# Kernel optimization log

Hardware: AMD Instinct MI355X
Metric: run time of the kernel (lower is better)

Reference implementation:

```python
import jax, jax.numpy as jnp
import numpy as np

EPS = 1e-12  # torch F.normalize eps
SIGMA_RBF = 1.0  # rbf bandwidth (init arg sigma=1)


def _l2norm(v, axis=-1):
    return v / jnp.maximum(jnp.linalg.norm(v, axis=axis, keepdims=True), EPS)


def setup_inputs() -> dict:
    key = jax.random.key(0)
    kx, kw, kb, ku, kc = jax.random.split(key, 5)
    B, C, E, F = 512, 100, 2048, 128
    x = jax.random.normal(kx, (B, E), dtype=jnp.float32)
    # per-class Linear weights [C, F, E] and biases [C, F] (torch Linear layout: out x in)
    bound = 1.0 / np.sqrt(E)
    W = jax.random.uniform(kw, (C, F, E), minval=-bound, maxval=bound, dtype=jnp.float32)
    b = jax.random.uniform(kb, (C, F), minval=-bound, maxval=bound, dtype=jnp.float32)
    # spectral-norm power-iteration vectors u (one per class, normalized)
    u = _l2norm(jax.random.normal(ku, (C, F), dtype=jnp.float32))
    # centroid buffer c (EMA means; randn stand-in for a trained state)
    c = jax.random.normal(kc, (C, F), dtype=jnp.float32)
    return {"x": x, "W": W, "b": b, "u": u, "c": c}


def reference(x, W, b, u, c):
    # --- spectral norm: one power-iteration step per class (torch default) ---
    v = _l2norm(jnp.einsum('cfe,cf->ce', W, u))        # v = normalize(W^T u)  [C,E]
    u2 = _l2norm(jnp.einsum('cfe,ce->cf', W, v))       # u = normalize(W v)    [C,F]
    sigma = jnp.einsum('cf,cfe,ce->c', u2, W, v)       # sigma = u^T W v       [C]
    Wn = W / sigma[:, None, None]
    # --- fused per-class linear projections: z[b,c,f] ---
    z = jnp.einsum('be,cfe->bcf', x, Wn) + b[None, :, :]
    # --- RBF to centroids: exp(-||c - z||^2 / (2 sigma^2)) ---
    dist2 = jnp.sum((c[None, :, :] - z) ** 2, axis=-1)  # [B, C]
    probs = jnp.exp(-dist2 / (2.0 * SIGMA_RBF ** 2))
    return probs
```

## Files before the change

### kernel.cpp

```cpp
#include <hip/hip_runtime.h>
#include <math.h>

#define B_ 512
#define C_ 100
#define E_ 2048
#define F_ 128
#define NCHUNK 16
#define CHUNKW 128

typedef _Float16 f16x8 __attribute__((ext_vector_type(8)));
typedef float    f32x4 __attribute__((ext_vector_type(4)));

#define AS1q __attribute__((address_space(1)))
#define AS3q __attribute__((address_space(3)))

__device__ __forceinline__ void gl_lds16(const void* g, void* lds_base) {
    __builtin_amdgcn_global_load_lds((const AS1q void*)g, (AS3q void*)lds_base, 16, 0, 0);
}

__global__ __launch_bounds__(256, 3)
void k_gram(const float* __restrict__ W, _Float16* __restrict__ Wh,
            const float* __restrict__ x, _Float16* __restrict__ xh,
            const float* __restrict__ u, float* __restrict__ ychunks) {
    const int b = blockIdx.x;
    const int t = threadIdx.x;

    if (b >= 1600) {
        const size_t base = (size_t)(b - 1600) * 32768 + t * 8;
#pragma unroll
        for (int it = 0; it < 16; ++it) {
            const size_t idx = base + (size_t)it * 2048;
            float4 a  = *(const float4*)(x + idx);
            float4 bb = *(const float4*)(x + idx + 4);
            f16x8 h;
            h[0] = (_Float16)a.x;  h[1] = (_Float16)a.y;  h[2] = (_Float16)a.z;  h[3] = (_Float16)a.w;
            h[4] = (_Float16)bb.x; h[5] = (_Float16)bb.y; h[6] = (_Float16)bb.z; h[7] = (_Float16)bb.w;
            *(f16x8*)(xh + idx) = h;
        }
        return;
    }

    const int c     = b >> 4;
    const int chunk = b & 15;
    const int w  = t >> 6;
    const int l  = t & 63;
    const int wm = w & 1, wn = w >> 1;
    const int ln = l & 15, quad = l >> 4;

    __shared__ _Float16 Ts[128 * 64];

    f32x4 acc[4][4];
#pragma unroll
    for (int mt = 0; mt < 4; ++mt)
#pragma unroll
        for (int nt = 0; nt < 4; ++nt) acc[mt][nt] = (f32x4){0.f, 0.f, 0.f, 0.f};

    const int r  = t >> 1;
    const int cb = (t & 1) * 32;
    const float* wsrc = W  + ((size_t)c * F_ + r) * E_ + cb;
    _Float16*    wdst = Wh + ((size_t)c * F_ + r) * E_ + cb;
    const int kbase = chunk * CHUNKW;

    float4 f[8];
#pragma unroll
    for (int j = 0; j < 8; ++j) f[j] = *(const float4*)(wsrc + kbase + j * 4);

#pragma unroll
    for (int i = 0; i < CHUNKW / 64; ++i) {
        const int k0 = kbase + i * 64;
        f16x8 h[4];
#pragma unroll
        for (int j = 0; j < 4; ++j) {
            h[j][0] = (_Float16)f[2*j].x;   h[j][1] = (_Float16)f[2*j].y;
            h[j][2] = (_Float16)f[2*j].z;   h[j][3] = (_Float16)f[2*j].w;
            h[j][4] = (_Float16)f[2*j+1].x; h[j][5] = (_Float16)f[2*j+1].y;
            h[j][6] = (_Float16)f[2*j+1].z; h[j][7] = (_Float16)f[2*j+1].w;
        }
        __syncthreads();
#pragma unroll
        for (int j = 0; j < 4; ++j) {
            const int g = (cb >> 3) + j;
            *(f16x8*)&Ts[r * 64 + ((g ^ (r & 7)) << 3)] = h[j];
        }
        __syncthreads();

#pragma unroll
        for (int j = 0; j < 4; ++j) *(f16x8*)(wdst + k0 + j * 8) = h[j];
        if (i + 1 < CHUNKW / 64) {
#pragma unroll
            for (int j = 0; j < 8; ++j) f[j] = *(const float4*)(wsrc + k0 + 64 + j * 4);
        }

#pragma unroll
        for (int kk = 0; kk < 64; kk += 32) {
            const int g0 = (kk >> 3) + quad;
            const int sw = (g0 ^ (ln & 7)) * 8;
            f16x8 av[4], bv[4];
#pragma unroll
            for (int mt = 0; mt < 4; ++mt)
                av[mt] = *(const f16x8*)&Ts[(wm * 64 + mt * 16 + ln) * 64 + sw];
#pragma unroll
            for (int nt = 0; nt < 4; ++nt)
                bv[nt] = *(const f16x8*)&Ts[(wn * 64 + nt * 16 + ln) * 64 + sw];
#pragma unroll
            for (int mt = 0; mt < 4; ++mt)
#pragma unroll
                for (int nt = 0; nt < 4; ++nt)
                    acc[mt][nt] = __builtin_amdgcn_mfma_f32_16x16x32_f16(
                        av[mt], bv[nt], acc[mt][nt], 0, 0, 0);
        }
    }

    const float* uc = u + (size_t)c * F_;
    float un[4];
#pragma unroll
    for (int nt = 0; nt < 4; ++nt) un[nt] = uc[wn * 64 + nt * 16 + ln];

    __syncthreads();
    float* red = (float*)&Ts[0];

#pragma unroll
    for (int mt = 0; mt < 4; ++mt) {
#pragma unroll
        for (int rr = 0; rr < 4; ++rr) {
            float py = acc[mt][0][rr] * un[0];
            py = fmaf(acc[mt][1][rr], un[1], py);
            py = fmaf(acc[mt][2][rr], un[2], py);
            py = fmaf(acc[mt][3][rr], un[3], py);
            py += __shfl_xor(py, 1, 64);
            py += __shfl_xor(py, 2, 64);
            py += __shfl_xor(py, 4, 64);
            py += __shfl_xor(py, 8, 64);
            if (ln == 0) {
                int m = wm * 64 + mt * 16 + quad * 4 + rr;
                red[m * 2 + wn] = py;
            }
        }
    }
    __syncthreads();
    if (t < 128) {
        float yv = red[t * 2] + red[t * 2 + 1];
        ychunks[((size_t)chunk * C_ + c) * F_ + t] = yv;
    }
}

__global__ __launch_bounds__(256, 2)
void k_main(const _Float16* __restrict__ xh, const _Float16* __restrict__ Wh,
            const float* __restrict__ bias, const float* __restrict__ cent,
            const float* __restrict__ u, const float* __restrict__ ychunks,
            float* __restrict__ out) {
    const int c  = blockIdx.y;
    const int b0 = blockIdx.x * 128;
    const int t  = threadIdx.x;
    const int w  = t >> 6;
    const int l  = t & 63;
    const int wm = w & 1, wn = w >> 1;
    const int ln = l & 15, quad = l >> 4;

    __shared__ _Float16 Xs[128 * 64];
    __shared__ _Float16 Ws[128 * 64];
    __shared__ float red2[2][2];
    __shared__ float s_rsig;

    if (t < 128) {
        float yf = 0.f;
#pragma unroll
        for (int ch = 0; ch < NCHUNK; ++ch)
            yf += ychunks[((size_t)ch * C_ + c) * F_ + t];
        float nvp = u[(size_t)c * F_ + t] * yf;
        float tsp = yf * yf;
        for (int off = 32; off; off >>= 1) {
            nvp += __shfl_down(nvp, off, 64);
            tsp += __shfl_down(tsp, off, 64);
        }
        if (l == 0) { red2[w][0] = nvp; red2[w][1] = tsp; }
    }
    __syncthreads();
    if (t == 0) s_rsig = sqrtf((red2[0][0] + red2[1][0]) / (red2[0][1] + red2[1][1]));

    f32x4 acc[4][4];
#pragma unroll
    for (int mt = 0; mt < 4; ++mt)
#pragma unroll
        for (int nt = 0; nt < 4; ++nt) acc[mt][nt] = (f32x4){0.f, 0.f, 0.f, 0.f};

    const int lr = l >> 3;
    const int lg = (l & 7) ^ lr;
    const _Float16* xsrc = xh + (size_t)(b0 + w * 32 + lr) * E_ + lg * 8;
    const _Float16* wsrc = Wh + ((size_t)c * F_ + w * 32 + lr) * E_ + lg * 8;

    for (int k0 = 0; k0 < E_; k0 += 64) {
#pragma unroll
        for (int q = 0; q < 4; ++q)
            gl_lds16(xsrc + (size_t)q * 8 * E_ + k0, &Xs[(w * 4 + q) * 512]);
#pragma unroll
        for (int q = 0; q < 4; ++q)
            gl_lds16(wsrc + (size_t)q * 8 * E_ + k0, &Ws[(w * 4 + q) * 512]);
        __syncthreads();

#pragma unroll
        for (int kk = 0; kk < 64; kk += 32) {
            const int g0 = (kk >> 3) + quad;
            const int sw = (g0 ^ (ln & 7)) * 8;
            f16x8 av[4], bv[4];
#pragma unroll
            for (int mt = 0; mt < 4; ++mt)
                av[mt] = *(const f16x8*)&Xs[(wm * 64 + mt * 16 + ln) * 64 + sw];
#pragma unroll
            for (int nt = 0; nt < 4; ++nt)
                bv[nt] = *(const f16x8*)&Ws[(wn * 64 + nt * 16 + ln) * 64 + sw];
#pragma unroll
            for (int mt = 0; mt < 4; ++mt)
#pragma unroll
                for (int nt = 0; nt < 4; ++nt)
                    acc[mt][nt] = __builtin_amdgcn_mfma_f32_16x16x32_f16(
                        av[mt], bv[nt], acc[mt][nt], 0, 0, 0);
        }
        __syncthreads();
    }

    const float rsigma = s_rsig;

    float bi[4], ce[4];
#pragma unroll
    for (int nt = 0; nt < 4; ++nt) {
        int f = wn * 64 + nt * 16 + ln;
        bi[nt] = bias[c * F_ + f];
        ce[nt] = cent[c * F_ + f];
    }

    float* red = (float*)&Xs[0];

#pragma unroll
    for (int mt = 0; mt < 4; ++mt) {
#pragma unroll
        for (int r = 0; r < 4; ++r) {
            float part = 0.f;
#pragma unroll
            for (int nt = 0; nt < 4; ++nt) {
                float z = fmaf(acc[mt][nt][r], rsigma, bi[nt]);
                float d = ce[nt] - z;
                part = fmaf(d, d, part);
            }
            part += __shfl_xor(part, 1, 64);
            part += __shfl_xor(part, 2, 64);
            part += __shfl_xor(part, 4, 64);
            part += __shfl_xor(part, 8, 64);
            if (ln == 0) {
                int m = wm * 64 + mt * 16 + quad * 4 + r;
                red[m * 2 + wn] = part;
            }
        }
    }
    __syncthreads();
    if (t < 128) {
        float d2 = red[t * 2] + red[t * 2 + 1];
        out[(size_t)(b0 + t) * C_ + c] = expf(-0.5f * d2);
    }
}

extern "C" void kernel_launch(void* const* d_in, const int* in_sizes, int n_in,
                              void* d_out, int out_size, void* d_ws, size_t ws_size,
                              hipStream_t stream) {
    const float* x  = (const float*)d_in[0];
    const float* W  = (const float*)d_in[1];
    const float* b  = (const float*)d_in[2];
    const float* u  = (const float*)d_in[3];
    const float* cc = (const float*)d_in[4];
    float* out = (float*)d_out;

    char* ws = (char*)d_ws;
    _Float16* Wh      = (_Float16*)ws;
    _Float16* xh      = (_Float16*)(ws + (size_t)C_ * F_ * E_ * 2);
    float*    ychunks = (float*)(ws + (size_t)C_ * F_ * E_ * 2 + (size_t)B_ * E_ * 2);

    k_gram<<<1632, 256, 0, stream>>>(W, Wh, x, xh, u, ychunks);

    dim3 grid(B_ / 128, C_);
    k_main<<<grid, 256, 0, stream>>>(xh, Wh, b, cc, u, ychunks, out);
}
```

Baseline: 218.2 us.

## Drop fp16 staging copies; load fp32 into LDS and convert per fragment

Removes the intermediate fp16 copies of W and x. Both kernels now stream fp32 data straight into LDS with async global-to-LDS loads and convert to fp16 when building MFMA fragments. This avoids writing and re-reading the fp16 buffers and removes the conversion blocks from the gram kernel. In exchange, LDS tiles double in size, LDS read traffic doubles, and the main kernel now reads fp32 W per batch tile, which doubles its global bytes unless the cache absorbs them.

```diff
diff --git a/kernel.cpp b/kernel.cpp
--- a/kernel.cpp
+++ b/kernel.cpp
@@ -18,36 +18,31 @@
     __builtin_amdgcn_global_load_lds((const AS1q void*)g, (AS3q void*)lds_base, 16, 0, 0);
 }
 
+__device__ __forceinline__ f16x8 frag_ld(const float* T, int r, int p) {
+    const int k = r & 15;
+    const int b = r << 6;
+    const f32x4 lo = *(const f32x4*)&T[b + ((((p << 1))     ^ k) << 2)];
+    const f32x4 hi = *(const f32x4*)&T[b + ((((p << 1) | 1) ^ k) << 2)];
+    f16x8 fr;
+    fr[0] = (_Float16)lo[0]; fr[1] = (_Float16)lo[1];
+    fr[2] = (_Float16)lo[2]; fr[3] = (_Float16)lo[3];
+    fr[4] = (_Float16)hi[0]; fr[5] = (_Float16)hi[1];
+    fr[6] = (_Float16)hi[2]; fr[7] = (_Float16)hi[3];
+    return fr;
+}
+
 __global__ __launch_bounds__(256, 3)
-void k_gram(const float* __restrict__ W, _Float16* __restrict__ Wh,
-            const float* __restrict__ x, _Float16* __restrict__ xh,
-            const float* __restrict__ u, float* __restrict__ ychunks) {
-    const int b = blockIdx.x;
-    const int t = threadIdx.x;
-
-    if (b >= 1600) {
-        const size_t base = (size_t)(b - 1600) * 32768 + t * 8;
-#pragma unroll
-        for (int it = 0; it < 16; ++it) {
-            const size_t idx = base + (size_t)it * 2048;
-            float4 a  = *(const float4*)(x + idx);
-            float4 bb = *(const float4*)(x + idx + 4);
-            f16x8 h;
-            h[0] = (_Float16)a.x;  h[1] = (_Float16)a.y;  h[2] = (_Float16)a.z;  h[3] = (_Float16)a.w;
-            h[4] = (_Float16)bb.x; h[5] = (_Float16)bb.y; h[6] = (_Float16)bb.z; h[7] = (_Float16)bb.w;
-            *(f16x8*)(xh + idx) = h;
-        }
-        return;
-    }
-
-    const int c     = b >> 4;
-    const int chunk = b & 15;
+void k_gram(const float* __restrict__ W, const float* __restrict__ u,
+            float* __restrict__ ychunks) {
+    const int chunk = blockIdx.x;
+    const int c     = blockIdx.y;
+    const int t  = threadIdx.x;
     const int w  = t >> 6;
     const int l  = t & 63;
     const int wm = w & 1, wn = w >> 1;
     const int ln = l & 15, quad = l >> 4;
 
-    __shared__ _Float16 Ts[128 * 64];
+    __shared__ float Ts[128 * 64];
 
     f32x4 acc[4][4];
 #pragma unroll
@@ -55,53 +50,31 @@
 #pragma unroll
         for (int nt = 0; nt < 4; ++nt) acc[mt][nt] = (f32x4){0.f, 0.f, 0.f, 0.f};
 
-    const int r  = t >> 1;
-    const int cb = (t & 1) * 32;
-    const float* wsrc = W  + ((size_t)c * F_ + r) * E_ + cb;
-    _Float16*    wdst = Wh + ((size_t)c * F_ + r) * E_ + cb;
-    const int kbase = chunk * CHUNKW;
-
-    float4 f[8];
-#pragma unroll
-    for (int j = 0; j < 8; ++j) f[j] = *(const float4*)(wsrc + kbase + j * 4);
-
-#pragma unroll
-    for (int i = 0; i < CHUNKW / 64; ++i) {
-        const int k0 = kbase + i * 64;
-        f16x8 h[4];
-#pragma unroll
-        for (int j = 0; j < 4; ++j) {
-            h[j][0] = (_Float16)f[2*j].x;   h[j][1] = (_Float16)f[2*j].y;
-            h[j][2] = (_Float16)f[2*j].z;   h[j][3] = (_Float16)f[2*j].w;
-            h[j][4] = (_Float16)f[2*j+1].x; h[j][5] = (_Float16)f[2*j+1].y;
-            h[j][6] = (_Float16)f[2*j+1].z; h[j][7] = (_Float16)f[2*j+1].w;
-        }
-        __syncthreads();
-#pragma unroll
-        for (int j = 0; j < 4; ++j) {
-            const int g = (cb >> 3) + j;
-            *(f16x8*)&Ts[r * 64 + ((g ^ (r & 7)) << 3)] = h[j];
-        }
-        __syncthreads();
-
-#pragma unroll
-        for (int j = 0; j < 4; ++j) *(f16x8*)(wdst + k0 + j * 8) = h[j];
-        if (i + 1 < CHUNKW / 64) {
-#pragma unroll
-            for (int j = 0; j < 8; ++j) f[j] = *(const float4*)(wsrc + k0 + 64 + j * 4);
-        }
+    const int lrow4 = l >> 4, cs = l & 15;
+    const float* wbase = W + (size_t)c * F_ * E_ + chunk * CHUNKW;
+
+#pragma unroll
+    for (int it = 0; it < CHUNKW / 64; ++it) {
+        const int k0 = it * 64;
+#pragma unroll
+        for (int qq = 0; qq < 8; ++qq) {
+            const int q   = w * 8 + qq;
+            const int r   = q * 4 + lrow4;
+            const int off = ((cs ^ (r & 15)) << 2);
+            gl_lds16(wbase + (size_t)r * E_ + k0 + off, &Ts[q * 256]);
+        }
+        __syncthreads();
 
 #pragma unroll
         for (int kk = 0; kk < 64; kk += 32) {
-            const int g0 = (kk >> 3) + quad;
-            const int sw = (g0 ^ (ln & 7)) * 8;
+            const int pb = quad + (kk >> 3);
             f16x8 av[4], bv[4];
 #pragma unroll
             for (int mt = 0; mt < 4; ++mt)
-                av[mt] = *(const f16x8*)&Ts[(wm * 64 + mt * 16 + ln) * 64 + sw];
+                av[mt] = frag_ld(Ts, wm * 64 + mt * 16 + ln, pb);
 #pragma unroll
             for (int nt = 0; nt < 4; ++nt)
-                bv[nt] = *(const f16x8*)&Ts[(wn * 64 + nt * 16 + ln) * 64 + sw];
+                bv[nt] = frag_ld(Ts, wn * 64 + nt * 16 + ln, pb);
 #pragma unroll
             for (int mt = 0; mt < 4; ++mt)
 #pragma unroll
@@ -109,6 +82,7 @@
                     acc[mt][nt] = __builtin_amdgcn_mfma_f32_16x16x32_f16(
                         av[mt], bv[nt], acc[mt][nt], 0, 0, 0);
         }
+        __syncthreads();
     }
 
     const float* uc = u + (size_t)c * F_;
@@ -116,7 +90,6 @@
 #pragma unroll
     for (int nt = 0; nt < 4; ++nt) un[nt] = uc[wn * 64 + nt * 16 + ln];
 
-    __syncthreads();
     float* red = (float*)&Ts[0];
 
 #pragma unroll
@@ -145,7 +118,7 @@
 }
 
 __global__ __launch_bounds__(256, 2)
-void k_main(const _Float16* __restrict__ xh, const _Float16* __restrict__ Wh,
+void k_main(const float* __restrict__ x, const float* __restrict__ W,
             const float* __restrict__ bias, const float* __restrict__ cent,
             const float* __restrict__ u, const float* __restrict__ ychunks,
             float* __restrict__ out) {
@@ -157,8 +130,8 @@
     const int wm = w & 1, wn = w >> 1;
     const int ln = l & 15, quad = l >> 4;
 
-    __shared__ _Float16 Xs[128 * 64];
-    __shared__ _Float16 Ws[128 * 64];
+    __shared__ float Xs[128 * 64];
+    __shared__ float Ws[128 * 64];
     __shared__ float red2[2][2];
     __shared__ float s_rsig;
 
@@ -184,31 +157,31 @@
 #pragma unroll
         for (int nt = 0; nt < 4; ++nt) acc[mt][nt] = (f32x4){0.f, 0.f, 0.f, 0.f};
 
-    const int lr = l >> 3;
-    const int lg = (l & 7) ^ lr;
-    const _Float16* xsrc = xh + (size_t)(b0 + w * 32 + lr) * E_ + lg * 8;
-    const _Float16* wsrc = Wh + ((size_t)c * F_ + w * 32 + lr) * E_ + lg * 8;
+    const int lrow4 = l >> 4, cs = l & 15;
+    const float* xbase = x + (size_t)b0 * E_;
+    const float* wbase = W + (size_t)c * F_ * E_;
 
     for (int k0 = 0; k0 < E_; k0 += 64) {
 #pragma unroll
-        for (int q = 0; q < 4; ++q)
-            gl_lds16(xsrc + (size_t)q * 8 * E_ + k0, &Xs[(w * 4 + q) * 512]);
-#pragma unroll
-        for (int q = 0; q < 4; ++q)
-            gl_lds16(wsrc + (size_t)q * 8 * E_ + k0, &Ws[(w * 4 + q) * 512]);
+        for (int qq = 0; qq < 8; ++qq) {
+            const int q   = w * 8 + qq;
+            const int r   = q * 4 + lrow4;
+            const int off = ((cs ^ (r & 15)) << 2);
+            gl_lds16(xbase + (size_t)r * E_ + k0 + off, &Xs[q * 256]);
+            gl_lds16(wbase + (size_t)r * E_ + k0 + off, &Ws[q * 256]);
+        }
         __syncthreads();
 
 #pragma unroll
         for (int kk = 0; kk < 64; kk += 32) {
-            const int g0 = (kk >> 3) + quad;
-            const int sw = (g0 ^ (ln & 7)) * 8;
+            const int pb = quad + (kk >> 3);
             f16x8 av[4], bv[4];
 #pragma unroll
             for (int mt = 0; mt < 4; ++mt)
-                av[mt] = *(const f16x8*)&Xs[(wm * 64 + mt * 16 + ln) * 64 + sw];
+                av[mt] = frag_ld(Xs, wm * 64 + mt * 16 + ln, pb);
 #pragma unroll
             for (int nt = 0; nt < 4; ++nt)
-                bv[nt] = *(const f16x8*)&Ws[(wn * 64 + nt * 16 + ln) * 64 + sw];
+                bv[nt] = frag_ld(Ws, wn * 64 + nt * 16 + ln, pb);
 #pragma unroll
             for (int mt = 0; mt < 4; ++mt)
 #pragma unroll
@@ -269,13 +242,11 @@
     const float* cc = (const float*)d_in[4];
     float* out = (float*)d_out;
 
-    char* ws = (char*)d_ws;
-    _Float16* Wh      = (_Float16*)ws;
-    _Float16* xh      = (_Float16*)(ws + (size_t)C_ * F_ * E_ * 2);
-    float*    ychunks = (float*)(ws + (size_t)C_ * F_ * E_ * 2 + (size_t)B_ * E_ * 2);
-
-    k_gram<<<1632, 256, 0, stream>>>(W, Wh, x, xh, u, ychunks);
+    float* ychunks = (float*)d_ws;
+
+    dim3 ggrid(NCHUNK, C_);
+    k_gram<<<ggrid, 256, 0, stream>>>(W, u, ychunks);
 
     dim3 grid(B_ / 128, C_);
-    k_main<<<grid, 256, 0, stream>>>(xh, Wh, b, cc, u, ychunks, out);
-}
+    k_main<<<grid, 256, 0, stream>>>(x, W, b, cc, u, ychunks, out);
+}
```

Measured after the change: 246.9 us. +13.2%, slower.

## Stage fp32 W tiles via direct global-to-LDS loads in gram kernel

Applied to the files above, without the earlier changes.

The gram kernel now loads fp32 W chunks straight into LDS with global_load_lds and an XOR swizzle, instead of loading through registers, converting to fp16, and then writing to LDS. Fragments are converted to fp16 when read from LDS, both for the MFMA operands and for the fp16 copy of W written back to global memory. This removes register staging and the register prefetch, but it doubles the LDS tile to 32KB, adds conversion work on every fragment read, and adds a barrier per iteration. Separately, k_main's launch bounds are raised to 3 blocks per SM, which may add register pressure.

```diff
diff --git a/kernel.cpp b/kernel.cpp
--- a/kernel.cpp
+++ b/kernel.cpp
@@ -16,6 +16,19 @@
 
 __device__ __forceinline__ void gl_lds16(const void* g, void* lds_base) {
     __builtin_amdgcn_global_load_lds((const AS1q void*)g, (AS3q void*)lds_base, 16, 0, 0);
+}
+
+__device__ __forceinline__ f16x8 frag_ld(const float* T, int r, int p) {
+    const int k = r & 15;
+    const int b = r << 6;
+    const f32x4 lo = *(const f32x4*)&T[b + ((((p << 1))     ^ k) << 2)];
+    const f32x4 hi = *(const f32x4*)&T[b + ((((p << 1) | 1) ^ k) << 2)];
+    f16x8 fr;
+    fr[0] = (_Float16)lo[0]; fr[1] = (_Float16)lo[1];
+    fr[2] = (_Float16)lo[2]; fr[3] = (_Float16)lo[3];
+    fr[4] = (_Float16)hi[0]; fr[5] = (_Float16)hi[1];
+    fr[6] = (_Float16)hi[2]; fr[7] = (_Float16)hi[3];
+    return fr;
 }
 
 __global__ __launch_bounds__(256, 3)
@@ -47,7 +60,7 @@
     const int wm = w & 1, wn = w >> 1;
     const int ln = l & 15, quad = l >> 4;
 
-    __shared__ _Float16 Ts[128 * 64];
+    __shared__ float Ts[128 * 64];
 
     f32x4 acc[4][4];
 #pragma unroll
@@ -55,53 +68,52 @@
 #pragma unroll
         for (int nt = 0; nt < 4; ++nt) acc[mt][nt] = (f32x4){0.f, 0.f, 0.f, 0.f};
 
-    const int r  = t >> 1;
-    const int cb = (t & 1) * 32;
-    const float* wsrc = W  + ((size_t)c * F_ + r) * E_ + cb;
-    _Float16*    wdst = Wh + ((size_t)c * F_ + r) * E_ + cb;
-    const int kbase = chunk * CHUNKW;
-
-    float4 f[8];
-#pragma unroll
-    for (int j = 0; j < 8; ++j) f[j] = *(const float4*)(wsrc + kbase + j * 4);
-
-#pragma unroll
-    for (int i = 0; i < CHUNKW / 64; ++i) {
-        const int k0 = kbase + i * 64;
-        f16x8 h[4];
-#pragma unroll
-        for (int j = 0; j < 4; ++j) {
-            h[j][0] = (_Float16)f[2*j].x;   h[j][1] = (_Float16)f[2*j].y;
-            h[j][2] = (_Float16)f[2*j].z;   h[j][3] = (_Float16)f[2*j].w;
-            h[j][4] = (_Float16)f[2*j+1].x; h[j][5] = (_Float16)f[2*j+1].y;
-            h[j][6] = (_Float16)f[2*j+1].z; h[j][7] = (_Float16)f[2*j+1].w;
-        }
-        __syncthreads();
-#pragma unroll
-        for (int j = 0; j < 4; ++j) {
-            const int g = (cb >> 3) + j;
-            *(f16x8*)&Ts[r * 64 + ((g ^ (r & 7)) << 3)] = h[j];
-        }
-        __syncthreads();
-
-#pragma unroll
-        for (int j = 0; j < 4; ++j) *(f16x8*)(wdst + k0 + j * 8) = h[j];
-        if (i + 1 < CHUNKW / 64) {
-#pragma unroll
-            for (int j = 0; j < 8; ++j) f[j] = *(const float4*)(wsrc + k0 + 64 + j * 4);
+    const int lrow4 = l >> 4, cs = l & 15;
+    const float* wbase = W + (size_t)c * F_ * E_ + chunk * CHUNKW;
+
+    const int cr = t >> 1, cb = (t & 1) * 32;
+    _Float16* wdst = Wh + ((size_t)c * F_ + cr) * E_ + chunk * CHUNKW + cb;
+
+#pragma unroll
+    for (int it = 0; it < CHUNKW / 64; ++it) {
+        const int k0 = it * 64;
+#pragma unroll
+        for (int qq = 0; qq < 8; ++qq) {
+            const int q   = w * 8 + qq;
+            const int r   = q * 4 + lrow4;
+            const int off = ((cs ^ (r & 15)) << 2);
+            gl_lds16(wbase + (size_t)r * E_ + k0 + off, &Ts[q * 256]);
+        }
+        __syncthreads();
+
+        {
+            f32x4 v[8];
+#pragma unroll
+            for (int j = 0; j < 8; ++j) {
+                const int g = (cb >> 2) + j;
+                v[j] = *(const f32x4*)&Ts[cr * 64 + ((g ^ (cr & 15)) << 2)];
+            }
+#pragma unroll
+            for (int j = 0; j < 4; ++j) {
+                f16x8 h;
+                h[0] = (_Float16)v[2*j][0]; h[1] = (_Float16)v[2*j][1];
+                h[2] = (_Float16)v[2*j][2]; h[3] = (_Float16)v[2*j][3];
+                h[4] = (_Float16)v[2*j+1][0]; h[5] = (_Float16)v[2*j+1][1];
+                h[6] = (_Float16)v[2*j+1][2]; h[7] = (_Float16)v[2*j+1][3];
+                *(f16x8*)(wdst + k0 + j * 8) = h;
+            }
         }
 
 #pragma unroll
         for (int kk = 0; kk < 64; kk += 32) {
-            const int g0 = (kk >> 3) + quad;
-            const int sw = (g0 ^ (ln & 7)) * 8;
+            const int pb = quad + (kk >> 3);
             f16x8 av[4], bv[4];
 #pragma unroll
             for (int mt = 0; mt < 4; ++mt)
-                av[mt] = *(const f16x8*)&Ts[(wm * 64 + mt * 16 + ln) * 64 + sw];
+                av[mt] = frag_ld(Ts, wm * 64 + mt * 16 + ln, pb);
 #pragma unroll
             for (int nt = 0; nt < 4; ++nt)
-                bv[nt] = *(const f16x8*)&Ts[(wn * 64 + nt * 16 + ln) * 64 + sw];
+                bv[nt] = frag_ld(Ts, wn * 64 + nt * 16 + ln, pb);
 #pragma unroll
             for (int mt = 0; mt < 4; ++mt)
 #pragma unroll
@@ -109,6 +121,7 @@
                     acc[mt][nt] = __builtin_amdgcn_mfma_f32_16x16x32_f16(
                         av[mt], bv[nt], acc[mt][nt], 0, 0, 0);
         }
+        __syncthreads();
     }
 
     const float* uc = u + (size_t)c * F_;
@@ -116,7 +129,6 @@
 #pragma unroll
     for (int nt = 0; nt < 4; ++nt) un[nt] = uc[wn * 64 + nt * 16 + ln];
 
-    __syncthreads();
     float* red = (float*)&Ts[0];
 
 #pragma unroll
@@ -144,7 +156,7 @@
     }
 }
 
-__global__ __launch_bounds__(256, 2)
+__global__ __launch_bounds__(256, 3)
 void k_main(const _Float16* __restrict__ xh, const _Float16* __restrict__ Wh,
             const float* __restrict__ bias, const float* __restrict__ cent,
             const float* __restrict__ u, const float* __restrict__ ychunks,
```

Result: no change. 216.6 us (-0.8%).
